# Performance work log

Hardware: AMD Instinct MI355X
Metric: run time of the kernel (lower is better)

Reference implementation:

```python
import jax, jax.numpy as jnp
import numpy as np

BLANK = 0
BEAM = 5


def setup_inputs() -> dict:
    key = jax.random.key(0)
    ks = jax.random.split(key, 8)
    B, T, H, V = 8, 128, 1024, 4096
    s = lambda k, sh, sc: jax.random.normal(k, sh, dtype=jnp.float32) * sc
    return {
        "tn_output": s(ks[0], (B, T, H), 1.0),
        "E": s(ks[1], (V, H), 0.02),
        "W_ih": s(ks[2], (4 * H, H), 0.02),
        "W_hh": s(ks[3], (4 * H, H), 0.02),
        "b_lstm": jnp.zeros((4 * H,), jnp.float32),
        "W_tn": s(ks[4], (H, H), 0.02),
        "W_pn": s(ks[5], (H, H), 0.02),
        "b_joint": jnp.zeros((H,), jnp.float32),
        "W_out": s(ks[6], (H, V), 0.02),
        "b_out": jnp.zeros((V,), jnp.float32),
    }


def _beam_search(tn_output, E, W_ih, W_hh, b_lstm, W_tn, W_pn, b_joint, W_out, b_out):
    # Batched RNN-T beam search (one expansion per frame, all B*K hyps batched).
    B, T, H = tn_output.shape
    V = E.shape[0]
    K = BEAM
    NEG = jnp.float32(-1e9)

    tn_proj = jnp.einsum('bth,hd->btd', tn_output, W_tn)  # [B,T,H] precomputed

    tokens0 = jnp.full((B, K), BLANK, jnp.int32)          # last emitted token
    h0 = jnp.zeros((B, K, H), tn_output.dtype)
    c0 = jnp.zeros((B, K, H), tn_output.dtype)
    scores0 = jnp.full((B, K), NEG).at[:, 0].set(0.0)     # only beam 0 alive
    preds0 = jnp.zeros((B, K, T), jnp.int32)
    lens0 = jnp.zeros((B, K), jnp.int32)

    def step(carry, tn_t):  # tn_t: [B,H] (projected TN output at frame t)
        tokens, h, c, scores, preds, lens = carry
        # --- prediction network (LSTM cell) over all B*K hyps at once ---
        emb = E[tokens]                                   # [B,K,H]
        gates = emb @ W_ih.T + h @ W_hh.T + b_lstm        # [B,K,4H]
        i_g, f_g, g_g, o_g = jnp.split(gates, 4, axis=-1)
        c_new = jax.nn.sigmoid(f_g) * c + jax.nn.sigmoid(i_g) * jnp.tanh(g_g)
        h_new = jax.nn.sigmoid(o_g) * jnp.tanh(c_new)     # [B,K,H]
        # --- joint network ---
        joint = jnp.tanh(tn_t[:, None, :] + h_new @ W_pn + b_joint)
        logp = jax.nn.log_softmax(joint @ W_out + b_out, axis=-1)  # [B,K,V]
        # --- beam expand + prune ---
        cand = (scores[:, :, None] + logp).reshape(B, K * V)
        top_s, top_i = jax.lax.top_k(cand, K)             # [B,K]
        parent = top_i // V
        tok = (top_i % V).astype(jnp.int32)
        is_blank = tok == BLANK

        g2 = lambda x: jnp.take_along_axis(x, parent, axis=1)
        g3 = lambda x: jnp.take_along_axis(x, parent[:, :, None], axis=1)
        # blank keeps the parent's pre-step decoder state; non-blank advances it
        h_next = jnp.where(is_blank[:, :, None], g3(h), g3(h_new))
        c_next = jnp.where(is_blank[:, :, None], g3(c), g3(c_new))
        tokens_next = jnp.where(is_blank, g2(tokens), tok)
        lens_p = g2(lens)
        preds_p = g3(preds.reshape(B, K, -1)).reshape(B, K, preds.shape[-1])
        pos = (jnp.arange(preds.shape[-1])[None, None, :] == lens_p[:, :, None]) & (~is_blank)[:, :, None]
        preds_next = jnp.where(pos, tok[:, :, None], preds_p)
        lens_next = lens_p + (~is_blank).astype(jnp.int32)
        return (tokens_next, h_next, c_next, top_s, preds_next, lens_next), None

    carry, _ = jax.lax.scan(step, (tokens0, h0, c0, scores0, preds0, lens0),
                            jnp.swapaxes(tn_proj, 0, 1))
    _, _, _, scores, preds, lens = carry
    # original normalizes by len(prediction) which includes the leading blank -> lens+1
    norm = scores / (lens.astype(scores.dtype) + 1.0)
    return preds, lens, norm


def reference(tn_output, E, W_ih, W_hh, b_lstm, W_tn, W_pn, b_joint, W_out, b_out):
    preds, lens, norm = _beam_search(tn_output, E, W_ih, W_hh, b_lstm,
                                     W_tn, W_pn, b_joint, W_out, b_out)
    best = jnp.argmax(norm, axis=1)                       # [B]
    best_preds = jnp.take_along_axis(preds, best[:, None, None], axis=1)[:, 0]  # [B,T]
    best_lens = jnp.take_along_axis(lens, best[:, None], axis=1)[:, 0]          # [B]
    mean_score = jnp.exp(jnp.max(norm, axis=1)).mean()
    return best_preds, best_lens, mean_score, norm
```

## Files before the change

kernel.cpp:

```cpp
#include <hip/hip_runtime.h>
#include <math.h>

#define HH 1024
#define VV 4096
#define TSTEPS 128
#define NB 256
#define NT 512

typedef float  floatx4 __attribute__((ext_vector_type(4)));
typedef int    intx4   __attribute__((ext_vector_type(4)));

#define GLL(gp, lp, aux) __builtin_amdgcn_global_load_lds( \
    (const __attribute__((address_space(1))) unsigned int*)(gp), \
    (__attribute__((address_space(3))) unsigned int*)(lp), 16, 0, aux)


__device__ __forceinline__ float sigf(float x) { return 1.0f / (1.0f + expf(-x)); }

__device__ __forceinline__ float rowsum16(float x) {
  x += __int_as_float(__builtin_amdgcn_update_dpp(0, __float_as_int(x), 0x111, 0xf, 0xf, true));
  x += __int_as_float(__builtin_amdgcn_update_dpp(0, __float_as_int(x), 0x112, 0xf, 0xf, true));
  x += __int_as_float(__builtin_amdgcn_update_dpp(0, __float_as_int(x), 0x114, 0xf, 0xf, true));
  x += __int_as_float(__builtin_amdgcn_update_dpp(0, __float_as_int(x), 0x118, 0xf, 0xf, true));
  return x;
}

__device__ __forceinline__ void ins5(float* bv, int* bi, float v, int i) {
#pragma unroll
  for (int j = 0; j < 5; ++j) {
    if (v > bv[j] || (v == bv[j] && i < bi[j])) {
#pragma unroll
      for (int s = 4; s > j; --s) { bv[s] = bv[s - 1]; bi[s] = bi[s - 1]; }
      bv[j] = v; bi[j] = i;
      break;
    }
  }
}


__device__ __forceinline__ float ldcc(const float* p) {
  float v;
  asm volatile("global_load_dword %0, %1, off sc0 sc1\n\ts_waitcnt vmcnt(0)"
               : "=&v"(v) : "v"(p) : "memory");
  return v;
}
__device__ __forceinline__ int ldcci(const int* p) {
  int v;
  asm volatile("global_load_dword %0, %1, off sc0 sc1\n\ts_waitcnt vmcnt(0)"
               : "=&v"(v) : "v"(p) : "memory");
  return v;
}
__device__ __forceinline__ floatx4 ldcc4(const float* p) {
  floatx4 v;
  asm volatile("global_load_dwordx4 %0, %1, off sc0 sc1\n\ts_waitcnt vmcnt(0)"
               : "=&v"(v) : "v"(p) : "memory");
  return v;
}
__device__ __forceinline__ void stcc(float* p, float v) {
  asm volatile("global_store_dword %0, %1, off sc0 sc1" :: "v"(p), "v"(v) : "memory");
}
__device__ __forceinline__ void stcci(int* p, int v) {
  asm volatile("global_store_dword %0, %1, off sc0 sc1" :: "v"(p), "v"(v) : "memory");
}
__device__ __forceinline__ void stcc4(float* p, floatx4 v) {
  asm volatile("global_store_dwordx4 %0, %1, off sc0 sc1" :: "v"(p), "v"(v) : "memory");
}
__device__ __forceinline__ void stcc4i(int* p, intx4 v) {
  asm volatile("global_store_dwordx4 %0, %1, off sc0 sc1" :: "v"(p), "v"(v) : "memory");
}

__device__ __forceinline__ void ldwt(floatx4& v, const float* p) {
  asm volatile("global_load_dwordx4 %0, %1, off\n\ts_waitcnt vmcnt(0)"
               : "=&v"(v) : "v"(p));
}

__device__ __forceinline__ void ldcc_top5(const float* pv, const int* pi,
                                          float tv[5], int ti[5]) {
  floatx4 a; float a1; intx4 b; int b1;
  asm volatile(
      "global_load_dwordx4 %0, %4, off sc0 sc1\n\t"
      "global_load_dword   %1, %5, off sc0 sc1\n\t"
      "global_load_dwordx4 %2, %6, off sc0 sc1\n\t"
      "global_load_dword   %3, %7, off sc0 sc1\n\t"
      "s_waitcnt vmcnt(0)"
      : "=&v"(a), "=&v"(a1), "=&v"(b), "=&v"(b1)
      : "v"(pv), "v"(pv + 4), "v"(pi), "v"(pi + 4)
      : "memory");
  tv[0] = a.x; tv[1] = a.y; tv[2] = a.z; tv[3] = a.w; tv[4] = a1;
  ti[0] = b.x; ti[1] = b.y; ti[2] = b.z; ti[3] = b.w; ti[4] = b1;
}

__device__ __forceinline__ void ldcc_state(const float* ps, const int* pl, const int* pt,
                                           const int* pp, const int* pb,
                                           float& sc, int& ln, int& tk, int& pr, int& bl) {
  asm volatile(
      "global_load_dword %0, %5, off sc0 sc1\n\t"
      "global_load_dword %1, %6, off sc0 sc1\n\t"
      "global_load_dword %2, %7, off sc0 sc1\n\t"
      "global_load_dword %3, %8, off sc0 sc1\n\t"
      "global_load_dword %4, %9, off sc0 sc1\n\t"
      "s_waitcnt vmcnt(0)"
      : "=&v"(sc), "=&v"(ln), "=&v"(tk), "=&v"(pr), "=&v"(bl)
      : "v"(ps), "v"(pl), "v"(pt), "v"(pp), "v"(pb)
      : "memory");
}


__global__ __launch_bounds__(256) void k_transp(const float* __restrict__ in,
                                                float* __restrict__ out, int R, int C) {
  __shared__ float tile[32][33];
  int c0 = blockIdx.x * 32, r0 = blockIdx.y * 32;
  int tx = threadIdx.x & 31, ty = threadIdx.x >> 5;
#pragma unroll
  for (int i = 0; i < 32; i += 8) tile[ty + i][tx] = in[(long)(r0 + ty + i) * C + c0 + tx];
  __syncthreads();
#pragma unroll
  for (int i = 0; i < 32; i += 8) out[(long)(c0 + ty + i) * R + r0 + tx] = tile[tx][ty + i];
}

__global__ __launch_bounds__(256) void k_tnproj(const float* __restrict__ A,
                                                const float* __restrict__ B,
                                                float* __restrict__ C) {
  __shared__ float As[64][20];
  __shared__ float Bs[16][68];
  int tid = threadIdx.x, blk = blockIdx.x;
  int bx = blk & 15, by = blk >> 4;
  int tx = tid & 15, ty = tid >> 4;
  float acc[4][4];
#pragma unroll
  for (int i = 0; i < 4; i++)
#pragma unroll
    for (int j = 0; j < 4; j++) acc[i][j] = 0.f;
  for (int k0 = 0; k0 < 1024; k0 += 16) {
    {
      int row = tid >> 2, q = tid & 3;
      float4 v = *(const float4*)&A[(long)(by * 64 + row) * 1024 + k0 + q * 4];
      As[row][q * 4] = v.x; As[row][q * 4 + 1] = v.y; As[row][q * 4 + 2] = v.z; As[row][q * 4 + 3] = v.w;
    }
    {
      int row = tid >> 4, q = tid & 15;
      float4 v = *(const float4*)&B[(long)(k0 + row) * 1024 + bx * 64 + q * 4];
      *(float4*)&Bs[row][q * 4] = v;
    }
    __syncthreads();
#pragma unroll
    for (int kk = 0; kk < 16; kk++) {
      float a0 = As[ty * 4][kk], a1 = As[ty * 4 + 1][kk], a2 = As[ty * 4 + 2][kk], a3 = As[ty * 4 + 3][kk];
      float4 b4 = *(const float4*)&Bs[kk][tx * 4];
      acc[0][0] += a0 * b4.x; acc[0][1] += a0 * b4.y; acc[0][2] += a0 * b4.z; acc[0][3] += a0 * b4.w;
      acc[1][0] += a1 * b4.x; acc[1][1] += a1 * b4.y; acc[1][2] += a1 * b4.z; acc[1][3] += a1 * b4.w;
      acc[2][0] += a2 * b4.x; acc[2][1] += a2 * b4.y; acc[2][2] += a2 * b4.z; acc[2][3] += a2 * b4.w;
      acc[3][0] += a3 * b4.x; acc[3][1] += a3 * b4.y; acc[3][2] += a3 * b4.z; acc[3][3] += a3 * b4.w;
    }
    __syncthreads();
  }
#pragma unroll
  for (int i = 0; i < 4; i++) {
    float4 v = make_float4(acc[i][0], acc[i][1], acc[i][2], acc[i][3]);
    *(float4*)&C[(long)(by * 64 + ty * 4 + i) * 1024 + bx * 64 + tx * 4] = v;
  }
}


__global__ __launch_bounds__(NT, 1) void k_beam(
    const float* __restrict__ E, const float* __restrict__ Wih,
    const float* __restrict__ Whh, const float* __restrict__ b_lstm,
    const float* __restrict__ tn_proj, const float* __restrict__ WpnT,
    const float* __restrict__ b_joint, const float* __restrict__ WoutT,
    const float* __restrict__ b_out,
    float* __restrict__ h_pre0, float* __restrict__ h_pre1,
    float* __restrict__ c_pre0, float* __restrict__ c_pre1,
    float* __restrict__ h_new0, float* __restrict__ h_new1,
    float* __restrict__ c_new0, float* __restrict__ c_new1,
    float* __restrict__ joint, float* __restrict__ expsum_part,
    float* __restrict__ top5v, int* __restrict__ top5i,
    int* __restrict__ preds0, int* __restrict__ preds1,
    float* __restrict__ gscores, int* __restrict__ glens,
    int* __restrict__ gtokens, int* __restrict__ gpar, int* __restrict__ gblank,
    unsigned int* bar, float* __restrict__ out) {
  int tid = threadIdx.x, blk = blockIdx.x;
  int wav = tid >> 6, lane = tid & 63;

  __shared__ float xs[3 * 10240];
  __shared__ float part[640];
  __shared__ float s_scores[40], s_scls[5];
  __shared__ int s_tokens[40], s_lens[40], s_par[40], s_blank[40];
  __shared__ float s_csel[160];
  __shared__ float wtv[40];
  __shared__ int wti[40];
  __shared__ int s_best[8];
  __shared__ float s_maxn[8];

  floatx4 wihr[2][4], whhr[2][4], wpnr[4], woutr[2][4];
#pragma unroll
  for (int rr = 0; rr < 2; ++rr) {
    int gr = wav * 2 + rr;
    int jg = blk * 4 + (gr >> 2), g = gr & 3;
#pragma unroll
    for (int c = 0; c < 4; ++c) {
      ldwt(wihr[rr][c], &Wih[(long)(g * HH + jg) * HH + c * 256 + lane * 4]);
      ldwt(whhr[rr][c], &Whh[(long)(g * HH + jg) * HH + c * 256 + lane * 4]);
    }
  }
  {
    int d = blk * 4 + (wav >> 1);
#pragma unroll
    for (int c = 0; c < 4; ++c)
      ldwt(wpnr[c], &WpnT[(long)d * HH + c * 256 + lane * 4]);
  }
#pragma unroll
  for (int r = 0; r < 2; ++r) {
    int v = blk * 16 + wav * 2 + r;
#pragma unroll
    for (int c = 0; c < 4; ++c)
      ldwt(woutr[r][c], &WoutT[(long)v * HH + c * 256 + lane * 4]);
  }

  if (tid < 40) {
    s_scores[tid] = ((tid % 5) == 0) ? 0.f : -1e9f;
    s_tokens[tid] = 0; s_lens[tid] = 0; s_par[tid] = tid; s_blank[tid] = 1;
  }
  __syncthreads();

  unsigned int round = 0;
  auto gsync = [&]() {
    asm volatile("s_waitcnt vmcnt(0)" ::: "memory");
    __syncthreads();
    if (tid == 0)
      __hip_atomic_fetch_add(&bar[(blk & 15) * 16], 1u, __ATOMIC_RELAXED, __HIP_MEMORY_SCOPE_AGENT);
    ++round;
    if (tid < 16) {
      unsigned int tgt = round * 16u;
      while (__hip_atomic_load(&bar[tid * 16], __ATOMIC_RELAXED, __HIP_MEMORY_SCOPE_AGENT) < tgt)
        __builtin_amdgcn_s_sleep(2);
    }
    __syncthreads();
  };

  auto preds_update = [&](int u) {
    const int* pip = ((u - 1) & 1) ? preds1 : preds0;
    int* pop = (u & 1) ? preds1 : preds0;
    int m0 = blk * 10;
    for (int cell = tid; cell < 1280; cell += NT) {
      int j = cell >> 7, pos = cell & 127, gj = m0 + j;
      int isb = s_blank[gj];
      int plen = s_lens[gj] - (isb ? 0 : 1);
      int v = ldcci(&pip[s_par[gj] * 128 + pos]);
      if (!isb && pos == plen) v = s_tokens[gj];
      stcci(&pop[gj * 128 + pos], v);
    }
  };

  int mat = tid >> 8, k4f = (tid & 255) * 4;

  for (int t = 0; t < TSTEPS; ++t) {
    const float* h_pre_in = (t & 1) ? h_pre1 : h_pre0;
    const float* h_new_in = (t & 1) ? h_new1 : h_new0;
    const float* c_pre_in = (t & 1) ? c_pre1 : c_pre0;
    const float* c_new_in = (t & 1) ? c_new1 : c_new0;
    float* h_pre_o = (t & 1) ? h_pre0 : h_pre1;
    float* h_new_o = (t & 1) ? h_new0 : h_new1;
    float* c_pre_o = (t & 1) ? c_pre0 : c_pre1;
    float* c_new_o = (t & 1) ? c_new0 : c_new1;

    if (t > 0) {
      if (tid < 40) {
        float sc; int ln, tk, pr, bl;
        ldcc_state(&gscores[tid], &glens[tid], &gtokens[tid], &gpar[tid], &gblank[tid],
                   sc, ln, tk, pr, bl);
        s_scores[tid] = sc; s_lens[tid] = ln; s_tokens[tid] = tk;
        s_par[tid] = pr; s_blank[tid] = bl;
      }
      __syncthreads();
      if (tid < 160) {
        int mg = tid >> 2, j = tid & 3;
        const float* cb = s_blank[mg] ? c_pre_in : c_new_in;
        s_csel[tid] = ldcc(&cb[(long)s_par[mg] * HH + blk * 4 + j]);
      }
      if (blk < 4) {
        const int* pip = ((t - 1) & 1) ? preds1 : preds0;
        int* pop = (t & 1) ? preds1 : preds0;
        int m0b = blk * 10;
        int jA = tid >> 7, pA = tid & 127, gA = m0b + jA;
        int cB = tid + 512, jB = cB >> 7, pB = cB & 127, gB = m0b + jB;
        int cC = tid + 1024, jC = cC >> 7, pC = cC & 127, gC = m0b + jC;
        const int* aA = &pip[s_par[gA] * 128 + pA];
        const int* aB = &pip[s_par[gB] * 128 + pB];
        int vA, vB, vC = 0;
        if (tid < 256) {
          const int* aC = &pip[s_par[gC] * 128 + pC];
          asm volatile(
              "global_load_dword %0, %3, off sc0 sc1\n\t"
              "global_load_dword %1, %4, off sc0 sc1\n\t"
              "global_load_dword %2, %5, off sc0 sc1\n\t"
              "s_waitcnt vmcnt(0)"
              : "=&v"(vA), "=&v"(vB), "=&v"(vC)
              : "v"(aA), "v"(aB), "v"(aC) : "memory");
        } else {
          asm volatile(
              "global_load_dword %0, %2, off sc0 sc1\n\t"
              "global_load_dword %1, %3, off sc0 sc1\n\t"
              "s_waitcnt vmcnt(0)"
              : "=&v"(vA), "=&v"(vB)
              : "v"(aA), "v"(aB) : "memory");
        }
        {
          int isb = s_blank[gA], plen = s_lens[gA] - (isb ? 0 : 1);
          if (!isb && pA == plen) vA = s_tokens[gA];
          stcci(&pop[gA * 128 + pA], vA);
        }
        {
          int isb = s_blank[gB], plen = s_lens[gB] - (isb ? 0 : 1);
          if (!isb && pB == plen) vB = s_tokens[gB];
          stcci(&pop[gB * 128 + pB], vB);
        }
        if (tid < 256) {
          int isb = s_blank[gC], plen = s_lens[gC] - (isb ? 0 : 1);
          if (!isb && pC == plen) vC = s_tokens[gC];
          stcci(&pop[gC * 128 + pC], vC);
        }
      }
    }

    {
      auto g_issue = [&](int cc) {
        int ch = (blk + cc) & 7, mbase = ch * 5;
        float* dst = xs + (cc % 3) * 10240;
        if (mat == 0) {
#pragma unroll
          for (int i = 0; i < 5; ++i)
            GLL(&E[(long)s_tokens[mbase + i] * HH + k4f], dst + i * 2048 + tid * 4, 0);
        } else if (t > 0) {
#pragma unroll
          for (int i = 0; i < 5; ++i) {
            int mg = mbase + i;
            const float* hb = s_blank[mg] ? h_pre_in : h_new_in;
            GLL(&hb[(long)s_par[mg] * HH + k4f], dst + i * 2048 + tid * 4, 17);
          }
        }
        __builtin_amdgcn_sched_barrier(0);
      };
      g_issue(0); g_issue(1); g_issue(2);
      for (int cc = 0; cc < 8; ++cc) {
        int ch = (blk + cc) & 7;
        int mbase = ch * 5;
        float4* xb = (float4*)(xs + (cc % 3) * 10240);
        if (cc < 6)      asm volatile("s_waitcnt vmcnt(10)" ::: "memory");
        else if (cc == 6) asm volatile("s_waitcnt vmcnt(5)" ::: "memory");
        else             asm volatile("s_waitcnt vmcnt(0)" ::: "memory");
        __builtin_amdgcn_sched_barrier(0);
        if (t == 0 && mat == 1) {
          floatx4 z = {0.f, 0.f, 0.f, 0.f};
#pragma unroll
          for (int i = 0; i < 5; ++i) {
            *(floatx4*)(xb + i * 512 + tid) = z;
            if (blk == ch) stcc4(&h_pre_o[(long)(mbase + i) * HH + k4f], z);
          }
        }
        __syncthreads();
        if (t > 0 && mat == 1 && blk == ch) {
#pragma unroll
          for (int i = 0; i < 5; ++i)
            stcc4(&h_pre_o[(long)(mbase + i) * HH + k4f], *(floatx4*)(xb + i * 512 + tid));
        }
        float acc[5][2];
#pragma unroll
        for (int m = 0; m < 5; ++m) { acc[m][0] = 0.f; acc[m][1] = 0.f; }
#pragma unroll
        for (int m = 0; m < 5; ++m) {
#pragma unroll
          for (int c = 0; c < 4; ++c) {
            float4 x = xb[m * 512 + c * 64 + lane];
#pragma unroll
            for (int rr = 0; rr < 2; ++rr) {
              floatx4 ww = wihr[rr][c];
              acc[m][rr] += x.x * ww.x; acc[m][rr] += x.y * ww.y;
              acc[m][rr] += x.z * ww.z; acc[m][rr] += x.w * ww.w;
            }
          }
#pragma unroll
          for (int c = 0; c < 4; ++c) {
            float4 x = xb[m * 512 + 256 + c * 64 + lane];
#pragma unroll
            for (int rr = 0; rr < 2; ++rr) {
              floatx4 ww = whhr[rr][c];
              acc[m][rr] += x.x * ww.x; acc[m][rr] += x.y * ww.y;
              acc[m][rr] += x.z * ww.z; acc[m][rr] += x.w * ww.w;
            }
          }
        }
#pragma unroll
        for (int m = 0; m < 5; ++m) {
          acc[m][0] = rowsum16(acc[m][0]);
          acc[m][1] = rowsum16(acc[m][1]);
        }
        if ((lane & 15) == 15) {
          int grp = lane >> 4;
#pragma unroll
          for (int m = 0; m < 5; ++m) {
            part[(wav * 4 + grp) * 10 + m * 2] = acc[m][0];
            part[(wav * 4 + grp) * 10 + m * 2 + 1] = acc[m][1];
          }
        }
        __syncthreads();
        if (tid < 20) {
          int mloc = tid >> 2, j = tid & 3;
          int mg = mbase + mloc, jglob = blk * 4 + j;
          float gi = 0.f, gf = 0.f, gg = 0.f, go = 0.f;
#pragma unroll
          for (int r = 0; r < 4; ++r) {
            gi += part[((j * 2) * 4 + r) * 10 + mloc * 2];
            gf += part[((j * 2) * 4 + r) * 10 + mloc * 2 + 1];
            gg += part[((j * 2 + 1) * 4 + r) * 10 + mloc * 2];
            go += part[((j * 2 + 1) * 4 + r) * 10 + mloc * 2 + 1];
          }
          gi += b_lstm[jglob]; gf += b_lstm[HH + jglob];
          gg += b_lstm[2 * HH + jglob]; go += b_lstm[3 * HH + jglob];
          float csel = (t == 0) ? 0.f : s_csel[mg * 4 + j];
          float cn = sigf(gf) * csel + sigf(gi) * tanhf(gg);
          float hn = sigf(go) * tanhf(cn);
          long o = (long)mg * HH + jglob;
          stcc(&h_new_o[o], hn); stcc(&c_new_o[o], cn); stcc(&c_pre_o[o], csel);
        }
        if (cc < 5) g_issue(cc + 3);
      }
    }
    gsync();

    {
      auto j_issue = [&](int cc) {
        int ch = (blk + cc) & 3, mbase = ch * 10;
        float* dst = xs + (cc % 3) * 10240;
#pragma unroll
        for (int i = 0; i < 5; ++i)
          GLL(&h_new_o[(long)(mbase + mat + 2 * i) * HH + k4f], dst + i * 2048 + tid * 4, 17);
        __builtin_amdgcn_sched_barrier(0);
      };
      j_issue(0); j_issue(1); j_issue(2);
      for (int cc = 0; cc < 4; ++cc) {
        int ch = (blk + cc) & 3;
        int mbase = ch * 10;
        float4* xb = (float4*)(xs + (cc % 3) * 10240);
        if (cc < 2)      asm volatile("s_waitcnt vmcnt(10)" ::: "memory");
        else if (cc == 2) asm volatile("s_waitcnt vmcnt(5)" ::: "memory");
        else             asm volatile("s_waitcnt vmcnt(0)" ::: "memory");
        __builtin_amdgcn_sched_barrier(0);
        __syncthreads();
        float accj[5];
#pragma unroll
        for (int m = 0; m < 5; ++m) accj[m] = 0.f;
        int mh = (wav & 1) * 5;
#pragma unroll
        for (int m = 0; m < 5; ++m) {
#pragma unroll
          for (int c = 0; c < 4; ++c) {
            float4 x = xb[(mh + m) * 256 + c * 64 + lane];
            floatx4 ww = wpnr[c];
            accj[m] += x.x * ww.x; accj[m] += x.y * ww.y;
            accj[m] += x.z * ww.z; accj[m] += x.w * ww.w;
          }
        }
#pragma unroll
        for (int m = 0; m < 5; ++m) accj[m] = rowsum16(accj[m]);
        if ((lane & 15) == 15) {
          int grp = lane >> 4;
#pragma unroll
          for (int m = 0; m < 5; ++m) part[(wav * 4 + grp) * 5 + m] = accj[m];
        }
        __syncthreads();
        if (tid < 40) {
          int mloc = tid >> 2, d = tid & 3;
          int wv = d * 2 + (mloc >= 5 ? 1 : 0), m5 = mloc % 5;
          float s = 0.f;
#pragma unroll
          for (int r = 0; r < 4; ++r) s += part[(wv * 4 + r) * 5 + m5];
          int mg = mbase + mloc, dglob = blk * 4 + d, b = mg / 5;
          stcc(&joint[(long)mg * HH + dglob],
               tanhf(s + tn_proj[((long)b * TSTEPS + t) * HH + dglob] + b_joint[dglob]));
        }
        if (cc < 1) j_issue(cc + 3);
      }
    }
    gsync();

    {
      auto l_issue = [&](int cc) {
        int ch = (blk + cc) & 3, mbase = ch * 10;
        float* dst = xs + (cc % 3) * 10240;
#pragma unroll
        for (int i = 0; i < 5; ++i)
          GLL(&joint[(long)(mbase + mat + 2 * i) * HH + k4f], dst + i * 2048 + tid * 4, 17);
        __builtin_amdgcn_sched_barrier(0);
      };
      l_issue(0); l_issue(1); l_issue(2);
      for (int cc = 0; cc < 4; ++cc) {
        int ch = (blk + cc) & 3;
        int mbase = ch * 10;
        float4* xb = (float4*)(xs + (cc % 3) * 10240);
        if (cc < 2)      asm volatile("s_waitcnt vmcnt(10)" ::: "memory");
        else if (cc == 2) asm volatile("s_waitcnt vmcnt(5)" ::: "memory");
        else             asm volatile("s_waitcnt vmcnt(0)" ::: "memory");
        __builtin_amdgcn_sched_barrier(0);
        __syncthreads();
        float accl[10][2];
#pragma unroll
        for (int m = 0; m < 10; ++m) { accl[m][0] = 0.f; accl[m][1] = 0.f; }
#pragma unroll
        for (int m = 0; m < 10; ++m)
#pragma unroll
          for (int c = 0; c < 4; ++c) {
            float4 x = xb[m * 256 + c * 64 + lane];
#pragma unroll
            for (int r = 0; r < 2; ++r) {
              floatx4 ww = woutr[r][c];
              accl[m][r] += x.x * ww.x; accl[m][r] += x.y * ww.y;
              accl[m][r] += x.z * ww.z; accl[m][r] += x.w * ww.w;
            }
          }
#pragma unroll
        for (int m = 0; m < 10; ++m) {
          accl[m][0] = rowsum16(accl[m][0]);
          accl[m][1] = rowsum16(accl[m][1]);
        }
        if ((lane & 15) == 15) {
          int grp = lane >> 4;
#pragma unroll
          for (int m = 0; m < 10; ++m) {
            part[(wav * 4 + grp) * 20 + m * 2] = accl[m][0];
            part[(wav * 4 + grp) * 20 + m * 2 + 1] = accl[m][1];
          }
        }
        __syncthreads();
        if (tid < 160) {
          int mloc = tid >> 4, vloc = tid & 15;
          int wv = vloc >> 1, rowr = vloc & 1;
          float s = 0.f;
#pragma unroll
          for (int r = 0; r < 4; ++r) s += part[(wv * 4 + r) * 20 + mloc * 2 + rowr];
          int v = blk * 16 + vloc, mg = mbase + mloc;
          float lg = s + b_out[v];
          float e = rowsum16(expf(lg));
          if ((tid & 15) == 15) stcc(&expsum_part[mg * 256 + blk], e);
          float cv = lg; int ci = (mg % 5) * 4096 + v;
          float tv[5]; int ti5[5];
#pragma unroll
          for (int r5 = 0; r5 < 5; ++r5) {
            float mv = cv; int mi = ci;
#pragma unroll
            for (int off2 = 1; off2 < 16; off2 <<= 1) {
              float ov = __shfl_xor(mv, off2, 16);
              int oi = __shfl_xor(mi, off2, 16);
              if (ov > mv || (ov == mv && oi < mi)) { mv = ov; mi = oi; }
            }
            if (cv == mv && ci == mi) cv = -3.0e38f;
            tv[r5] = mv; ti5[r5] = mi;
          }
          if ((tid & 15) == 0) {
            int toff = (mg * 256 + blk) * 8;
            floatx4 tvv = {tv[0], tv[1], tv[2], tv[3]};
            intx4 tiv = {ti5[0], ti5[1], ti5[2], ti5[3]};
            stcc4(&top5v[toff], tvv); stcc(&top5v[toff + 4], tv[4]);
            stcc4i(&top5i[toff], tiv); stcci(&top5i[toff + 4], ti5[4]);
          }
        }
        if (cc < 1) l_issue(cc + 3);
      }
    }
    gsync();

    if (blk < 8) {
      int b = blk;
      if (wav < 5) {
        int kp = wav;
        const float* ep = &expsum_part[(b * 5 + kp) * 256];
        floatx4 e4 = ldcc4(&ep[lane * 4]);
        float tl = ((e4.x + e4.y) + e4.z) + e4.w;
        part[kp * 64 + lane] = tl;
        if (lane == 0) {
          float ssum = 0.f;
          for (int i = 0; i < 64; ++i) ssum += part[kp * 64 + i];
          s_scls[kp] = s_scores[b * 5 + kp] - logf(ssum);
        }
      }
      __syncthreads();
      float bv[5]; int bi5[5];
#pragma unroll
      for (int q = 0; q < 5; ++q) { bv[q] = -3.0e38f; bi5[q] = 0x7fffffff; }
      for (int e = wav * 160 + lane; e < wav * 160 + 160; e += 64) {
        int kp = e >> 8, blkc = e & 255;
        float base = s_scls[kp];
        int off = ((b * 5 + kp) * 256 + blkc) * 8;
        float tv[5]; int ti5[5];
        ldcc_top5(&top5v[off], &top5i[off], tv, ti5);
#pragma unroll
        for (int q = 0; q < 5; ++q) ins5(bv, bi5, tv[q] + base, ti5[q]);
      }
      float myv = 0.f; int myi = 0;
#pragma unroll
      for (int r = 0; r < 5; ++r) {
        float mv = bv[0]; int mi = bi5[0];
#pragma unroll
        for (int off2 = 1; off2 < 64; off2 <<= 1) {
          float ov = __shfl_xor(mv, off2, 64);
          int oi = __shfl_xor(mi, off2, 64);
          if (ov > mv || (ov == mv && oi < mi)) { mv = ov; mi = oi; }
        }
        if (bv[0] == mv && bi5[0] == mi) {
          bv[0] = bv[1]; bi5[0] = bi5[1]; bv[1] = bv[2]; bi5[1] = bi5[2];
          bv[2] = bv[3]; bi5[2] = bi5[3]; bv[3] = bv[4]; bi5[3] = bi5[4];
          bv[4] = -3.0e38f; bi5[4] = 0x7fffffff;
        }
        if (lane == r) { myv = mv; myi = mi; }
      }
      if (lane < 5) { wtv[wav * 5 + lane] = myv; wti[wav * 5 + lane] = myi; }
      __syncthreads();
      if (wav == 0) {
        float cv = (lane < 40) ? wtv[lane] : -3.0e38f;
        int ci = (lane < 40) ? wti[lane] : 0x7fffffff;
#pragma unroll
        for (int r = 0; r < 5; ++r) {
          float mv = cv; int mi = ci;
#pragma unroll
          for (int off2 = 1; off2 < 64; off2 <<= 1) {
            float ov = __shfl_xor(mv, off2, 64);
            int oi = __shfl_xor(mi, off2, 64);
            if (ov > mv || (ov == mv && oi < mi)) { mv = ov; mi = oi; }
          }
          if (cv == mv && ci == mi) cv = -3.0e38f;
          if (lane == r) { myv = mv; myi = mi; }
        }
        if (lane < 5) {
          int kp = myi >> 12, tok = myi & 4095;
          int isb = (tok == 0) ? 1 : 0;
          int pg = b * 5 + kp, slot = b * 5 + lane;
          stcc(&gscores[slot], myv); stcci(&gpar[slot], pg); stcci(&gblank[slot], isb);
          stcci(&gtokens[slot], isb ? s_tokens[pg] : tok);
          stcci(&glens[slot], s_lens[pg] + (isb ? 0 : 1));
        }
      }
    }
    gsync();
  }

  if (tid < 40) {
    float sc; int ln, tk, pr, bl;
    ldcc_state(&gscores[tid], &glens[tid], &gtokens[tid], &gpar[tid], &gblank[tid],
               sc, ln, tk, pr, bl);
    s_scores[tid] = sc; s_lens[tid] = ln; s_tokens[tid] = tk;
    s_par[tid] = pr; s_blank[tid] = bl;
  }
  __syncthreads();
  if (blk < 4) preds_update(TSTEPS);
  gsync();

  if (blk == 0) {
    if (tid < 40) out[1033 + tid] = s_scores[tid] / (float)(s_lens[tid] + 1);
    if (tid < 8) {
      float bvn = -3.0e38f; int bk = 0;
      for (int k = 0; k < 5; ++k) {
        float n = s_scores[tid * 5 + k] / (float)(s_lens[tid * 5 + k] + 1);
        if (n > bvn) { bvn = n; bk = k; }
      }
      s_best[tid] = bk; s_maxn[tid] = bvn;
      out[1024 + tid] = (float)s_lens[tid * 5 + bk];
    }
    __syncthreads();
    if (tid == 0) {
      float s = 0.f;
      for (int b = 0; b < 8; ++b) s += expf(s_maxn[b]);
      out[1032] = s / 8.f;
    }
    for (int cI = tid; cI < 1024; cI += NT) {
      int b = cI >> 7, pos = cI & 127;
      out[cI] = (float)ldcci(&preds0[(b * 5 + s_best[b]) * 128 + pos]);
    }
  }
}


extern "C" void kernel_launch(void* const* d_in, const int* in_sizes, int n_in,
                              void* d_out, int out_size, void* d_ws, size_t ws_size,
                              hipStream_t stream) {
  const float* tn   = (const float*)d_in[0];
  const float* E    = (const float*)d_in[1];
  const float* Wih  = (const float*)d_in[2];
  const float* Whh  = (const float*)d_in[3];
  const float* bl   = (const float*)d_in[4];
  const float* Wtn  = (const float*)d_in[5];
  const float* Wpn  = (const float*)d_in[6];
  const float* bj   = (const float*)d_in[7];
  const float* Wout = (const float*)d_in[8];
  const float* bo   = (const float*)d_in[9];
  float* out = (float*)d_out;

  unsigned int* bar = (unsigned int*)d_ws;
  float* w = (float*)d_ws + 256;
  size_t off = 0;
  float* tn_proj = w + off; off += 1048576;
  float* WpnT    = w + off; off += 1048576;
  float* WoutT   = w + off; off += 4194304;
  float* joint   = w + off; off += 40960;
  float* expsum  = w + off; off += 10240;
  float* top5v   = w + off; off += 81920;
  float* h_pre0  = w + off; off += 40960;
  float* h_pre1  = w + off; off += 40960;
  float* c_pre0  = w + off; off += 40960;
  float* c_pre1  = w + off; off += 40960;
  float* h_new0  = w + off; off += 40960;
  float* h_new1  = w + off; off += 40960;
  float* c_new0  = w + off; off += 40960;
  float* c_new1  = w + off; off += 40960;
  float* gscores = w + off; off += 40;
  int* ib = (int*)(w + off);
  int* top5i   = ib; ib += 81920;
  int* preds0  = ib; ib += 5120;
  int* preds1  = ib; ib += 5120;
  int* glens   = ib; ib += 40;
  int* gtokens = ib; ib += 40;
  int* gpar    = ib; ib += 40;
  int* gblank  = ib; ib += 40;
  if (ws_size < (size_t)(256 + off + 92320) * 4) return;

  hipMemsetAsync(bar, 0, 1024, stream);
  hipMemsetAsync(preds0, 0, 5120 * sizeof(int), stream);
  k_transp<<<dim3(32, 32), 256, 0, stream>>>(Wpn, WpnT, 1024, 1024);
  k_transp<<<dim3(128, 32), 256, 0, stream>>>(Wout, WoutT, 1024, 4096);
  k_tnproj<<<256, 256, 0, stream>>>(tn, Wtn, tn_proj);

  void* args[] = { (void*)&E, (void*)&Wih, (void*)&Whh, (void*)&bl,
                   (void*)&tn_proj, (void*)&WpnT, (void*)&bj, (void*)&WoutT, (void*)&bo,
                   (void*)&h_pre0, (void*)&h_pre1, (void*)&c_pre0, (void*)&c_pre1,
                   (void*)&h_new0, (void*)&h_new1, (void*)&c_new0, (void*)&c_new1,
                   (void*)&joint, (void*)&expsum, (void*)&top5v, (void*)&top5i,
                   (void*)&preds0, (void*)&preds1, (void*)&gscores, (void*)&glens,
                   (void*)&gtokens, (void*)&gpar, (void*)&gblank,
                   (void*)&bar, (void*)&out };
  hipLaunchCooperativeKernel((void*)k_beam, dim3(NB), dim3(NT), args, 0, stream);
}
```

Measured before the change: 14.65 ms.

## Replace async LDS triple-buffering with batched register loads over chunk pairs

```diff
diff --git a/kernel.cpp b/kernel.cpp
--- a/kernel.cpp
+++ b/kernel.cpp
@@ -9,10 +9,6 @@
 
 typedef float  floatx4 __attribute__((ext_vector_type(4)));
 typedef int    intx4   __attribute__((ext_vector_type(4)));
-
-#define GLL(gp, lp, aux) __builtin_amdgcn_global_load_lds( \
-    (const __attribute__((address_space(1))) unsigned int*)(gp), \
-    (__attribute__((address_space(3))) unsigned int*)(lp), 16, 0, aux)
 
 
 __device__ __forceinline__ float sigf(float x) { return 1.0f / (1.0f + expf(-x)); }
@@ -74,20 +70,62 @@
                : "=&v"(v) : "v"(p));
 }
 
-__device__ __forceinline__ void ldcc_top5(const float* pv, const int* pi,
-                                          float tv[5], int ti[5]) {
-  floatx4 a; float a1; intx4 b; int b1;
+__device__ __forceinline__ void ldcc4x10(
+    const float* p0, const float* p1, const float* p2, const float* p3, const float* p4,
+    const float* p5, const float* p6, const float* p7, const float* p8, const float* p9,
+    floatx4& v0, floatx4& v1, floatx4& v2, floatx4& v3, floatx4& v4,
+    floatx4& v5, floatx4& v6, floatx4& v7, floatx4& v8, floatx4& v9) {
   asm volatile(
-      "global_load_dwordx4 %0, %4, off sc0 sc1\n\t"
-      "global_load_dword   %1, %5, off sc0 sc1\n\t"
-      "global_load_dwordx4 %2, %6, off sc0 sc1\n\t"
-      "global_load_dword   %3, %7, off sc0 sc1\n\t"
+      "global_load_dwordx4 %0, %10, off sc0 sc1\n\t"
+      "global_load_dwordx4 %1, %11, off sc0 sc1\n\t"
+      "global_load_dwordx4 %2, %12, off sc0 sc1\n\t"
+      "global_load_dwordx4 %3, %13, off sc0 sc1\n\t"
+      "global_load_dwordx4 %4, %14, off sc0 sc1\n\t"
+      "global_load_dwordx4 %5, %15, off sc0 sc1\n\t"
+      "global_load_dwordx4 %6, %16, off sc0 sc1\n\t"
+      "global_load_dwordx4 %7, %17, off sc0 sc1\n\t"
+      "global_load_dwordx4 %8, %18, off sc0 sc1\n\t"
+      "global_load_dwordx4 %9, %19, off sc0 sc1\n\t"
       "s_waitcnt vmcnt(0)"
-      : "=&v"(a), "=&v"(a1), "=&v"(b), "=&v"(b1)
-      : "v"(pv), "v"(pv + 4), "v"(pi), "v"(pi + 4)
+      : "=&v"(v0), "=&v"(v1), "=&v"(v2), "=&v"(v3), "=&v"(v4),
+        "=&v"(v5), "=&v"(v6), "=&v"(v7), "=&v"(v8), "=&v"(v9)
+      : "v"(p0), "v"(p1), "v"(p2), "v"(p3), "v"(p4),
+        "v"(p5), "v"(p6), "v"(p7), "v"(p8), "v"(p9)
       : "memory");
-  tv[0] = a.x; tv[1] = a.y; tv[2] = a.z; tv[3] = a.w; tv[4] = a1;
-  ti[0] = b.x; ti[1] = b.y; ti[2] = b.z; ti[3] = b.w; ti[4] = b1;
+}
+
+__device__ __forceinline__ void ldcc_top5x3(
+    const float* pv0, const int* pi0, const float* pv1, const int* pi1,
+    const float* pv2, const int* pi2,
+    float tv0[5], int ti0[5], float tv1[5], int ti1[5], float tv2[5], int ti2[5]) {
+  floatx4 a0, a1, a2; float x0, x1, x2; intx4 b0, b1, b2; int y0, y1, y2;
+  asm volatile(
+      "global_load_dwordx4 %0, %12, off sc0 sc1\n\t"
+      "global_load_dword   %1, %13, off sc0 sc1\n\t"
+      "global_load_dwordx4 %2, %14, off sc0 sc1\n\t"
+      "global_load_dword   %3, %15, off sc0 sc1\n\t"
+      "global_load_dwordx4 %4, %16, off sc0 sc1\n\t"
+      "global_load_dword   %5, %17, off sc0 sc1\n\t"
+      "global_load_dwordx4 %6, %18, off sc0 sc1\n\t"
+      "global_load_dword   %7, %19, off sc0 sc1\n\t"
+      "global_load_dwordx4 %8, %20, off sc0 sc1\n\t"
+      "global_load_dword   %9, %21, off sc0 sc1\n\t"
+      "global_load_dwordx4 %10, %22, off sc0 sc1\n\t"
+      "global_load_dword   %11, %23, off sc0 sc1\n\t"
+      "s_waitcnt vmcnt(0)"
+      : "=&v"(a0), "=&v"(x0), "=&v"(b0), "=&v"(y0),
+        "=&v"(a1), "=&v"(x1), "=&v"(b1), "=&v"(y1),
+        "=&v"(a2), "=&v"(x2), "=&v"(b2), "=&v"(y2)
+      : "v"(pv0), "v"(pv0 + 4), "v"(pi0), "v"(pi0 + 4),
+        "v"(pv1), "v"(pv1 + 4), "v"(pi1), "v"(pi1 + 4),
+        "v"(pv2), "v"(pv2 + 4), "v"(pi2), "v"(pi2 + 4)
+      : "memory");
+  tv0[0] = a0.x; tv0[1] = a0.y; tv0[2] = a0.z; tv0[3] = a0.w; tv0[4] = x0;
+  ti0[0] = b0.x; ti0[1] = b0.y; ti0[2] = b0.z; ti0[3] = b0.w; ti0[4] = y0;
+  tv1[0] = a1.x; tv1[1] = a1.y; tv1[2] = a1.z; tv1[3] = a1.w; tv1[4] = x1;
+  ti1[0] = b1.x; ti1[1] = b1.y; ti1[2] = b1.z; ti1[3] = b1.w; ti1[4] = y1;
+  tv2[0] = a2.x; tv2[1] = a2.y; tv2[2] = a2.z; tv2[3] = a2.w; tv2[4] = x2;
+  ti2[0] = b2.x; ti2[1] = b2.y; ti2[2] = b2.z; ti2[3] = b2.w; ti2[4] = y2;
 }
 
 __device__ __forceinline__ void ldcc_state(const float* ps, const int* pl, const int* pt,
@@ -181,8 +219,8 @@
   int tid = threadIdx.x, blk = blockIdx.x;
   int wav = tid >> 6, lane = tid & 63;
 
-  __shared__ float xs[3 * 10240];
-  __shared__ float part[640];
+  __shared__ float xs[2 * 10240];
+  __shared__ float part[1280];
   __shared__ float s_scores[40], s_scls[5];
   __shared__ int s_tokens[40], s_lens[40], s_par[40], s_blank[40];
   __shared__ float s_csel[160];
@@ -190,6 +228,7 @@
   __shared__ int wti[40];
   __shared__ int s_best[8];
   __shared__ float s_maxn[8];
+  float4* xs4 = (float4*)xs;
 
   floatx4 wihr[2][4], whhr[2][4], wpnr[4], woutr[2][4];
 #pragma unroll
@@ -323,47 +362,7 @@
     }
 
     {
-      auto g_issue = [&](int cc) {
-        int ch = (blk + cc) & 7, mbase = ch * 5;
-        float* dst = xs + (cc % 3) * 10240;
-        if (mat == 0) {
-#pragma unroll
-          for (int i = 0; i < 5; ++i)
-            GLL(&E[(long)s_tokens[mbase + i] * HH + k4f], dst + i * 2048 + tid * 4, 0);
-        } else if (t > 0) {
-#pragma unroll
-          for (int i = 0; i < 5; ++i) {
-            int mg = mbase + i;
-            const float* hb = s_blank[mg] ? h_pre_in : h_new_in;
-            GLL(&hb[(long)s_par[mg] * HH + k4f], dst + i * 2048 + tid * 4, 17);
-          }
-        }
-        __builtin_amdgcn_sched_barrier(0);
-      };
-      g_issue(0); g_issue(1); g_issue(2);
-      for (int cc = 0; cc < 8; ++cc) {
-        int ch = (blk + cc) & 7;
-        int mbase = ch * 5;
-        float4* xb = (float4*)(xs + (cc % 3) * 10240);
-        if (cc < 6)      asm volatile("s_waitcnt vmcnt(10)" ::: "memory");
-        else if (cc == 6) asm volatile("s_waitcnt vmcnt(5)" ::: "memory");
-        else             asm volatile("s_waitcnt vmcnt(0)" ::: "memory");
-        __builtin_amdgcn_sched_barrier(0);
-        if (t == 0 && mat == 1) {
-          floatx4 z = {0.f, 0.f, 0.f, 0.f};
-#pragma unroll
-          for (int i = 0; i < 5; ++i) {
-            *(floatx4*)(xb + i * 512 + tid) = z;
-            if (blk == ch) stcc4(&h_pre_o[(long)(mbase + i) * HH + k4f], z);
-          }
-        }
-        __syncthreads();
-        if (t > 0 && mat == 1 && blk == ch) {
-#pragma unroll
-          for (int i = 0; i < 5; ++i)
-            stcc4(&h_pre_o[(long)(mbase + i) * HH + k4f], *(floatx4*)(xb + i * 512 + tid));
-        }
-        float acc[5][2];
+      auto g_fma = [&](const float4* xb, float (&acc)[5][2]) {
 #pragma unroll
         for (int m = 0; m < 5; ++m) { acc[m][0] = 0.f; acc[m][1] = 0.f; }
 #pragma unroll
@@ -398,21 +397,64 @@
           int grp = lane >> 4;
 #pragma unroll
           for (int m = 0; m < 5; ++m) {
-            part[(wav * 4 + grp) * 10 + m * 2] = acc[m][0];
-            part[(wav * 4 + grp) * 10 + m * 2 + 1] = acc[m][1];
-          }
-        }
-        __syncthreads();
+          }
+        }
+      };
+      (void)g_fma;
+
+      auto g_pw = [&](float (&acc)[5][2], float* pbuf) {
+        if ((lane & 15) == 15) {
+          int grp = lane >> 4;
+#pragma unroll
+          for (int m = 0; m < 5; ++m) {
+            pbuf[(wav * 4 + grp) * 10 + m * 2] = acc[m][0];
+            pbuf[(wav * 4 + grp) * 10 + m * 2 + 1] = acc[m][1];
+          }
+        }
+      };
+      auto g_core = [&](const float4* xb, float (&acc)[5][2]) {
+#pragma unroll
+        for (int m = 0; m < 5; ++m) { acc[m][0] = 0.f; acc[m][1] = 0.f; }
+#pragma unroll
+        for (int m = 0; m < 5; ++m) {
+#pragma unroll
+          for (int c = 0; c < 4; ++c) {
+            float4 x = xb[m * 512 + c * 64 + lane];
+#pragma unroll
+            for (int rr = 0; rr < 2; ++rr) {
+              floatx4 ww = wihr[rr][c];
+              acc[m][rr] += x.x * ww.x; acc[m][rr] += x.y * ww.y;
+              acc[m][rr] += x.z * ww.z; acc[m][rr] += x.w * ww.w;
+            }
+          }
+#pragma unroll
+          for (int c = 0; c < 4; ++c) {
+            float4 x = xb[m * 512 + 256 + c * 64 + lane];
+#pragma unroll
+            for (int rr = 0; rr < 2; ++rr) {
+              floatx4 ww = whhr[rr][c];
+              acc[m][rr] += x.x * ww.x; acc[m][rr] += x.y * ww.y;
+              acc[m][rr] += x.z * ww.z; acc[m][rr] += x.w * ww.w;
+            }
+          }
+        }
+#pragma unroll
+        for (int m = 0; m < 5; ++m) {
+          acc[m][0] = rowsum16(acc[m][0]);
+          acc[m][1] = rowsum16(acc[m][1]);
+        }
+      };
+      auto g_finish = [&](int ch, const float* pbuf) {
         if (tid < 20) {
           int mloc = tid >> 2, j = tid & 3;
-          int mg = mbase + mloc, jglob = blk * 4 + j;
+          int mg = ch * 5 + mloc, jglob = blk * 4 + j;
           float gi = 0.f, gf = 0.f, gg = 0.f, go = 0.f;
 #pragma unroll
           for (int r = 0; r < 4; ++r) {
-            gi += part[((j * 2) * 4 + r) * 10 + mloc * 2];
-            gf += part[((j * 2) * 4 + r) * 10 + mloc * 2 + 1];
-            gg += part[((j * 2 + 1) * 4 + r) * 10 + mloc * 2];
-            go += part[((j * 2 + 1) * 4 + r) * 10 + mloc * 2 + 1];
+            gi += pbuf[((j * 2) * 4 + r) * 10 + mloc * 2];
+            gf += pbuf[((j * 2) * 4 + r) * 10 + mloc * 2 + 1];
+            gg += pbuf[((j * 2 + 1) * 4 + r) * 10 + mloc * 2];
+            go += pbuf[((j * 2 + 1) * 4 + r) * 10 + mloc * 2 + 1];
           }
           gi += b_lstm[jglob]; gf += b_lstm[HH + jglob];
           gg += b_lstm[2 * HH + jglob]; go += b_lstm[3 * HH + jglob];
@@ -422,31 +464,83 @@
           long o = (long)mg * HH + jglob;
           stcc(&h_new_o[o], hn); stcc(&c_new_o[o], cn); stcc(&c_pre_o[o], csel);
         }
-        if (cc < 5) g_issue(cc + 3);
+      };
+
+      for (int cc = 0; cc < 8; cc += 2) {
+        int chA = (blk + cc) & 7, chB = (blk + cc + 1) & 7;
+        int mbA = chA * 5, mbB = chB * 5;
+        float4* xbA = xs4;
+        float4* xbB = xs4 + 2560;
+        if (mat == 0) {
+#pragma unroll
+          for (int i = 0; i < 5; ++i)
+            xbA[i * 512 + tid] = *(const float4*)&E[(long)s_tokens[mbA + i] * HH + k4f];
+#pragma unroll
+          for (int i = 0; i < 5; ++i)
+            xbB[i * 512 + tid] = *(const float4*)&E[(long)s_tokens[mbB + i] * HH + k4f];
+        } else if (t == 0) {
+          floatx4 z = {0.f, 0.f, 0.f, 0.f};
+#pragma unroll
+          for (int i = 0; i < 5; ++i) {
+            *(floatx4*)(xbA + i * 512 + tid) = z;
+            *(floatx4*)(xbB + i * 512 + tid) = z;
+            if (blk == chA) stcc4(&h_pre_o[(long)(mbA + i) * HH + k4f], z);
+            if (blk == chB) stcc4(&h_pre_o[(long)(mbB + i) * HH + k4f], z);
+          }
+        } else {
+          const float* pA[5]; const float* pB[5];
+#pragma unroll
+          for (int i = 0; i < 5; ++i) {
+            int mgA = mbA + i, mgB = mbB + i;
+            pA[i] = &((s_blank[mgA] ? h_pre_in : h_new_in)[(long)s_par[mgA] * HH + k4f]);
+            pB[i] = &((s_blank[mgB] ? h_pre_in : h_new_in)[(long)s_par[mgB] * HH + k4f]);
+          }
+          floatx4 a0, a1, a2, a3, a4, b0, b1, b2, b3, b4;
+          ldcc4x10(pA[0], pA[1], pA[2], pA[3], pA[4],
+                   pB[0], pB[1], pB[2], pB[3], pB[4],
+                   a0, a1, a2, a3, a4, b0, b1, b2, b3, b4);
+          *(floatx4*)(xbA + 0 * 512 + tid) = a0;
+          *(floatx4*)(xbA + 1 * 512 + tid) = a1;
+          *(floatx4*)(xbA + 2 * 512 + tid) = a2;
+          *(floatx4*)(xbA + 3 * 512 + tid) = a3;
+          *(floatx4*)(xbA + 4 * 512 + tid) = a4;
+          *(floatx4*)(xbB + 0 * 512 + tid) = b0;
+          *(floatx4*)(xbB + 1 * 512 + tid) = b1;
+          *(floatx4*)(xbB + 2 * 512 + tid) = b2;
+          *(floatx4*)(xbB + 3 * 512 + tid) = b3;
+          *(floatx4*)(xbB + 4 * 512 + tid) = b4;
+          if (blk == chA) {
+            stcc4(&h_pre_o[(long)(mbA + 0) * HH + k4f], a0);
+            stcc4(&h_pre_o[(long)(mbA + 1) * HH + k4f], a1);
+            stcc4(&h_pre_o[(long)(mbA + 2) * HH + k4f], a2);
+            stcc4(&h_pre_o[(long)(mbA + 3) * HH + k4f], a3);
+            stcc4(&h_pre_o[(long)(mbA + 4) * HH + k4f], a4);
+          }
+          if (blk == chB) {
+            stcc4(&h_pre_o[(long)(mbB + 0) * HH + k4f], b0);
+            stcc4(&h_pre_o[(long)(mbB + 1) * HH + k4f], b1);
+            stcc4(&h_pre_o[(long)(mbB + 2) * HH + k4f], b2);
+            stcc4(&h_pre_o[(long)(mbB + 3) * HH + k4f], b3);
+            stcc4(&h_pre_o[(long)(mbB + 4) * HH + k4f], b4);
+          }
+        }
+        __syncthreads();
+        float accA[5][2];
+        g_core(xbA, accA);
+        g_pw(accA, part);
+        __syncthreads();
+        g_finish(chA, part);
+        float accB[5][2];
+        g_core(xbB, accB);
+        g_pw(accB, part + 640);
+        __syncthreads();
+        g_finish(chB, part + 640);
       }
     }
     gsync();
 
     {
-      auto j_issue = [&](int cc) {
-        int ch = (blk + cc) & 3, mbase = ch * 10;
-        float* dst = xs + (cc % 3) * 10240;
-#pragma unroll
-        for (int i = 0; i < 5; ++i)
-          GLL(&h_new_o[(long)(mbase + mat + 2 * i) * HH + k4f], dst + i * 2048 + tid * 4, 17);
-        __builtin_amdgcn_sched_barrier(0);
-      };
-      j_issue(0); j_issue(1); j_issue(2);
-      for (int cc = 0; cc < 4; ++cc) {
-        int ch = (blk + cc) & 3;
-        int mbase = ch * 10;
-        float4* xb = (float4*)(xs + (cc % 3) * 10240);
-        if (cc < 2)      asm volatile("s_waitcnt vmcnt(10)" ::: "memory");
-        else if (cc == 2) asm volatile("s_waitcnt vmcnt(5)" ::: "memory");
-        else             asm volatile("s_waitcnt vmcnt(0)" ::: "memory");
-        __builtin_amdgcn_sched_barrier(0);
-        __syncthreads();
-        float accj[5];
+      auto j_core = [&](const float4* xb, float (&accj)[5]) {
 #pragma unroll
         for (int m = 0; m < 5; ++m) accj[m] = 0.f;
         int mh = (wav & 1) * 5;
@@ -462,47 +556,70 @@
         }
 #pragma unroll
         for (int m = 0; m < 5; ++m) accj[m] = rowsum16(accj[m]);
+      };
+      auto j_pw = [&](float (&accj)[5], float* pbuf) {
         if ((lane & 15) == 15) {
           int grp = lane >> 4;
 #pragma unroll
-          for (int m = 0; m < 5; ++m) part[(wav * 4 + grp) * 5 + m] = accj[m];
-        }
-        __syncthreads();
+          for (int m = 0; m < 5; ++m) pbuf[(wav * 4 + grp) * 5 + m] = accj[m];
+        }
+      };
+      auto j_finish = [&](int mbase, const float* pbuf) {
         if (tid < 40) {
           int mloc = tid >> 2, d = tid & 3;
           int wv = d * 2 + (mloc >= 5 ? 1 : 0), m5 = mloc % 5;
           float s = 0.f;
 #pragma unroll
-          for (int r = 0; r < 4; ++r) s += part[(wv * 4 + r) * 5 + m5];
+          for (int r = 0; r < 4; ++r) s += pbuf[(wv * 4 + r) * 5 + m5];
           int mg = mbase + mloc, dglob = blk * 4 + d, b = mg / 5;
           stcc(&joint[(long)mg * HH + dglob],
                tanhf(s + tn_proj[((long)b * TSTEPS + t) * HH + dglob] + b_joint[dglob]));
         }
-        if (cc < 1) j_issue(cc + 3);
+      };
+      for (int cc = 0; cc < 4; cc += 2) {
+        int chA = (blk + cc) & 3, chB = (blk + cc + 1) & 3;
+        int mbA = chA * 10, mbB = chB * 10;
+        float4* xbA = xs4;
+        float4* xbB = xs4 + 2560;
+        floatx4 a0, a1, a2, a3, a4, b0, b1, b2, b3, b4;
+        ldcc4x10(&h_new_o[(long)(mbA + mat + 0) * HH + k4f],
+                 &h_new_o[(long)(mbA + mat + 2) * HH + k4f],
+                 &h_new_o[(long)(mbA + mat + 4) * HH + k4f],
+                 &h_new_o[(long)(mbA + mat + 6) * HH + k4f],
+                 &h_new_o[(long)(mbA + mat + 8) * HH + k4f],
+                 &h_new_o[(long)(mbB + mat + 0) * HH + k4f],
+                 &h_new_o[(long)(mbB + mat + 2) * HH + k4f],
+                 &h_new_o[(long)(mbB + mat + 4) * HH + k4f],
+                 &h_new_o[(long)(mbB + mat + 6) * HH + k4f],
+                 &h_new_o[(long)(mbB + mat + 8) * HH + k4f],
+                 a0, a1, a2, a3, a4, b0, b1, b2, b3, b4);
+        *(floatx4*)(xbA + 0 * 512 + tid) = a0;
+        *(floatx4*)(xbA + 1 * 512 + tid) = a1;
+        *(floatx4*)(xbA + 2 * 512 + tid) = a2;
+        *(floatx4*)(xbA + 3 * 512 + tid) = a3;
+        *(floatx4*)(xbA + 4 * 512 + tid) = a4;
+        *(floatx4*)(xbB + 0 * 512 + tid) = b0;
+        *(floatx4*)(xbB + 1 * 512 + tid) = b1;
+        *(floatx4*)(xbB + 2 * 512 + tid) = b2;
+        *(floatx4*)(xbB + 3 * 512 + tid) = b3;
+        *(floatx4*)(xbB + 4 * 512 + tid) = b4;
+        __syncthreads();
+        float accjA[5];
+        j_core(xbA, accjA);
+        j_pw(accjA, part);
+        __syncthreads();
+        j_finish(mbA, part);
+        float accjB[5];
+        j_core(xbB, accjB);
+        j_pw(accjB, part + 640);
+        __syncthreads();
+        j_finish(mbB, part + 640);
       }
     }
     gsync();
 
     {
-      auto l_issue = [&](int cc) {
-        int ch = (blk + cc) & 3, mbase = ch * 10;
-        float* dst = xs + (cc % 3) * 10240;
-#pragma unroll
-        for (int i = 0; i < 5; ++i)
-          GLL(&joint[(long)(mbase + mat + 2 * i) * HH + k4f], dst + i * 2048 + tid * 4, 17);
-        __builtin_amdgcn_sched_barrier(0);
-      };
-      l_issue(0); l_issue(1); l_issue(2);
-      for (int cc = 0; cc < 4; ++cc) {
-        int ch = (blk + cc) & 3;
-        int mbase = ch * 10;
-        float4* xb = (float4*)(xs + (cc % 3) * 10240);
-        if (cc < 2)      asm volatile("s_waitcnt vmcnt(10)" ::: "memory");
-        else if (cc == 2) asm volatile("s_waitcnt vmcnt(5)" ::: "memory");
-        else             asm volatile("s_waitcnt vmcnt(0)" ::: "memory");
-        __builtin_amdgcn_sched_barrier(0);
-        __syncthreads();
-        float accl[10][2];
+      auto l_core = [&](const float4* xb, float (&accl)[10][2]) {
 #pragma unroll
         for (int m = 0; m < 10; ++m) { accl[m][0] = 0.f; accl[m][1] = 0.f; }
 #pragma unroll
@@ -522,21 +639,24 @@
           accl[m][0] = rowsum16(accl[m][0]);
           accl[m][1] = rowsum16(accl[m][1]);
         }
+      };
+      auto l_pw = [&](float (&accl)[10][2], float* pbuf) {
         if ((lane & 15) == 15) {
           int grp = lane >> 4;
 #pragma unroll
           for (int m = 0; m < 10; ++m) {
-            part[(wav * 4 + grp) * 20 + m * 2] = accl[m][0];
-            part[(wav * 4 + grp) * 20 + m * 2 + 1] = accl[m][1];
-          }
-        }
-        __syncthreads();
+            pbuf[(wav * 4 + grp) * 20 + m * 2] = accl[m][0];
+            pbuf[(wav * 4 + grp) * 20 + m * 2 + 1] = accl[m][1];
+          }
+        }
+      };
+      auto l_finish = [&](int mbase, const float* pbuf) {
         if (tid < 160) {
           int mloc = tid >> 4, vloc = tid & 15;
           int wv = vloc >> 1, rowr = vloc & 1;
           float s = 0.f;
 #pragma unroll
-          for (int r = 0; r < 4; ++r) s += part[(wv * 4 + r) * 20 + mloc * 2 + rowr];
+          for (int r = 0; r < 4; ++r) s += pbuf[(wv * 4 + r) * 20 + mloc * 2 + rowr];
           int v = blk * 16 + vloc, mg = mbase + mloc;
           float lg = s + b_out[v];
           float e = rowsum16(expf(lg));
@@ -563,7 +683,45 @@
             stcc4i(&top5i[toff], tiv); stcci(&top5i[toff + 4], ti5[4]);
           }
         }
-        if (cc < 1) l_issue(cc + 3);
+      };
+      for (int cc = 0; cc < 4; cc += 2) {
+        int chA = (blk + cc) & 3, chB = (blk + cc + 1) & 3;
+        int mbA = chA * 10, mbB = chB * 10;
+        float4* xbA = xs4;
+        float4* xbB = xs4 + 2560;
+        floatx4 a0, a1, a2, a3, a4, b0, b1, b2, b3, b4;
+        ldcc4x10(&joint[(long)(mbA + mat + 0) * HH + k4f],
+                 &joint[(long)(mbA + mat + 2) * HH + k4f],
+                 &joint[(long)(mbA + mat + 4) * HH + k4f],
+                 &joint[(long)(mbA + mat + 6) * HH + k4f],
+                 &joint[(long)(mbA + mat + 8) * HH + k4f],
+                 &joint[(long)(mbB + mat + 0) * HH + k4f],
+                 &joint[(long)(mbB + mat + 2) * HH + k4f],
+                 &joint[(long)(mbB + mat + 4) * HH + k4f],
+                 &joint[(long)(mbB + mat + 6) * HH + k4f],
+                 &joint[(long)(mbB + mat + 8) * HH + k4f],
+                 a0, a1, a2, a3, a4, b0, b1, b2, b3, b4);
+        *(floatx4*)(xbA + 0 * 512 + tid) = a0;
+        *(floatx4*)(xbA + 1 * 512 + tid) = a1;
+        *(floatx4*)(xbA + 2 * 512 + tid) = a2;
+        *(floatx4*)(xbA + 3 * 512 + tid) = a3;
+        *(floatx4*)(xbA + 4 * 512 + tid) = a4;
+        *(floatx4*)(xbB + 0 * 512 + tid) = b0;
+        *(floatx4*)(xbB + 1 * 512 + tid) = b1;
+        *(floatx4*)(xbB + 2 * 512 + tid) = b2;
+        *(floatx4*)(xbB + 3 * 512 + tid) = b3;
+        *(floatx4*)(xbB + 4 * 512 + tid) = b4;
+        __syncthreads();
+        float acclA[10][2];
+        l_core(xbA, acclA);
+        l_pw(acclA, part);
+        __syncthreads();
+        l_finish(mbA, part);
+        float acclB[10][2];
+        l_core(xbB, acclB);
+        l_pw(acclB, part + 640);
+        __syncthreads();
+        l_finish(mbB, part + 640);
       }
     }
     gsync();
@@ -586,23 +744,40 @@
       float bv[5]; int bi5[5];
 #pragma unroll
       for (int q = 0; q < 5; ++q) { bv[q] = -3.0e38f; bi5[q] = 0x7fffffff; }
-      for (int e = wav * 160 + lane; e < wav * 160 + 160; e += 64) {
-        int kp = e >> 8, blkc = e & 255;
-        float base = s_scls[kp];
-        int off = ((b * 5 + kp) * 256 + blkc) * 8;
-        float tv[5]; int ti5[5];
-        ldcc_top5(&top5v[off], &top5i[off], tv, ti5);
-#pragma unroll
-        for (int q = 0; q < 5; ++q) ins5(bv, bi5, tv[q] + base, ti5[q]);
+      int e0 = wav * 160 + lane;
+      int kp0 = e0 >> 8, off0 = ((b * 5 + kp0) * 256 + (e0 & 255)) * 8;
+      int e1 = e0 + 64;
+      int kp1 = e1 >> 8, off1 = ((b * 5 + kp1) * 256 + (e1 & 255)) * 8;
+      int e2 = e0 + 128;
+      int kp2 = e2 >> 8, off2 = ((b * 5 + kp2) * 256 + (e2 & 255)) * 8;
+      bool has2 = (lane < 32);
+      int off2s = has2 ? off2 : off0;
+      float tv0[5], tv1[5], tv2[5]; int ti0[5], ti1[5], ti2[5];
+      ldcc_top5x3(&top5v[off0], &top5i[off0], &top5v[off1], &top5i[off1],
+                  &top5v[off2s], &top5i[off2s], tv0, ti0, tv1, ti1, tv2, ti2);
+      {
+        float base = s_scls[kp0];
+#pragma unroll
+        for (int q = 0; q < 5; ++q) ins5(bv, bi5, tv0[q] + base, ti0[q]);
+      }
+      {
+        float base = s_scls[kp1];
+#pragma unroll
+        for (int q = 0; q < 5; ++q) ins5(bv, bi5, tv1[q] + base, ti1[q]);
+      }
+      if (has2) {
+        float base = s_scls[kp2];
+#pragma unroll
+        for (int q = 0; q < 5; ++q) ins5(bv, bi5, tv2[q] + base, ti2[q]);
       }
       float myv = 0.f; int myi = 0;
 #pragma unroll
       for (int r = 0; r < 5; ++r) {
         float mv = bv[0]; int mi = bi5[0];
 #pragma unroll
-        for (int off2 = 1; off2 < 64; off2 <<= 1) {
-          float ov = __shfl_xor(mv, off2, 64);
-          int oi = __shfl_xor(mi, off2, 64);
+        for (int off2_ = 1; off2_ < 64; off2_ <<= 1) {
+          float ov = __shfl_xor(mv, off2_, 64);
+          int oi = __shfl_xor(mi, off2_, 64);
           if (ov > mv || (ov == mv && oi < mi)) { mv = ov; mi = oi; }
         }
         if (bv[0] == mv && bi5[0] == mi) {
@@ -621,9 +796,9 @@
         for (int r = 0; r < 5; ++r) {
           float mv = cv; int mi = ci;
 #pragma unroll
-          for (int off2 = 1; off2 < 64; off2 <<= 1) {
-            float ov = __shfl_xor(mv, off2, 64);
-            int oi = __shfl_xor(mi, off2, 64);
+          for (int off2_ = 1; off2_ < 64; off2_ <<= 1) {
+            float ov = __shfl_xor(mv, off2_, 64);
+            int oi = __shfl_xor(mi, off2_, 64);
             if (ov > mv || (ov == mv && oi < mi)) { mv = ov; mi = oi; }
           }
           if (cv == mv && ci == mi) cv = -3.0e38f;
```

Measured after the change: 13.08 ms. 10.7% less time.
